# Optimization experiments

Measured on AMD Instinct MI355X. Metric: run time of the kernel, lower is better.

## Reference

```python
import jax, jax.numpy as jnp
import numpy as np

N_NODES = 50000
N_EDGES = 600000
N_FEAT = 64
D = 128
N_GRAPHS = 1024
N_LAYERS = 4


def setup_inputs() -> dict:
    key = jax.random.key(0)
    ks = jax.random.split(key, 16)
    x = jax.random.normal(ks[0], (N_NODES, N_FEAT), dtype=jnp.float32)
    edge_index = jax.random.randint(ks[1], (2, N_EDGES), 0, N_NODES, dtype=jnp.int64)
    batch_index = jnp.sort(jax.random.randint(ks[2], (N_NODES,), 0, N_GRAPHS, dtype=jnp.int64))
    def lin(k, fan_in, fan_out):
        s = 1.0 / np.sqrt(fan_in)
        kw, kb = jax.random.split(k)
        w = jax.random.uniform(kw, (fan_in, fan_out), minval=-s, maxval=s, dtype=jnp.float32)
        b = jax.random.uniform(kb, (fan_out,), minval=-s, maxval=s, dtype=jnp.float32)
        return w, b
    w0, b0 = lin(ks[3], N_FEAT, D)
    w1, b1 = lin(ks[4], D, D)
    w2, b2 = lin(ks[5], D, D)
    w3, b3 = lin(ks[6], D, D)
    wp, bp = lin(ks[7], D, D)
    return {"x": x, "edge_index": edge_index, "batch_index": batch_index,
            "w0": w0, "b0": b0, "w1": w1, "b1": b1, "w2": w2, "b2": b2,
            "w3": w3, "b3": b3, "wp": wp, "bp": bp}


def _gin_layer(x, src, dst, w, b):
    # GINConv with eps=0: MLP(x_i + sum_{j in N(i)} x_j); MLP = Linear -> ReLU
    agg = jax.ops.segment_sum(x[src], dst, num_segments=N_NODES)
    return jax.nn.relu((x + agg) @ w + b)


def reference(x, edge_index, batch_index, w0, b0, w1, b1, w2, b2, w3, b3, wp, bp):
    src, dst = edge_index[0], edge_index[1]
    # first layer changes width 64 -> 128; agg happens in input width
    agg0 = jax.ops.segment_sum(x[src], dst, num_segments=N_NODES)
    h = jax.nn.relu((x + agg0) @ w0 + b0)
    for w, b in ((w1, b1), (w2, b2), (w3, b3)):
        h = _gin_layer(h, src, dst, w, b)
    # global mean pool per graph
    sums = jax.ops.segment_sum(h, batch_index, num_segments=N_GRAPHS)
    counts = jax.ops.segment_sum(jnp.ones((N_NODES,), dtype=h.dtype), batch_index, num_segments=N_GRAPHS)
    pooled = sums / jnp.maximum(counts, 1.0)[:, None]
    # post_mp: Linear -> ReLU (dropout identity at inference)
    return jax.nn.relu(pooled @ wp + bp)
```

## Files before the change

### kernel.cpp

```cpp
#include <hip/hip_runtime.h>
#include <hip/hip_fp16.h>


#define N_NODES  50000
#define N_EDGES  600000
#define N_FEAT   64
#define DIM      128
#define N_GRAPHS 1024
#define NC       7
#define CSH      13
#define TOT2     (N_NODES * NC)
#define SCH      2048
#define NBLK     ((TOT2 + SCH - 1) / SCH)
#define TPB      256
#define GT128    ((N_NODES + 127) / 128)

typedef _Float16 f16x8 __attribute__((ext_vector_type(8)));
typedef float    f32x4 __attribute__((ext_vector_type(4)));

#define CNTZ2 (TOT2 / 4)
#define XWORK (N_NODES * N_FEAT / 4)
#define PREP_TOTAL (CNTZ2 + XWORK + N_FEAT * DIM + 3 * DIM * DIM)

__global__ __launch_bounds__(TPB) void prep_k(
    const float* __restrict__ x, __half* __restrict__ xh,
    const float* __restrict__ w0, const float* __restrict__ w1,
    const float* __restrict__ w2, const float* __restrict__ w3,
    __half* __restrict__ Wt0, __half* __restrict__ Wt1,
    __half* __restrict__ Wt2, __half* __restrict__ Wt3,
    int* __restrict__ cnt2) {
  int i = blockIdx.x * TPB + threadIdx.x;
  if (i < CNTZ2) {
    *reinterpret_cast<int4*>(cnt2 + i * 4) = make_int4(0, 0, 0, 0);
    return;
  }
  i -= CNTZ2;
  if (i < XWORK) {
    float4 v = *reinterpret_cast<const float4*>(x + (size_t)i * 4);
    union { __half2 h2[2]; uint2 u; } pk;
    pk.h2[0] = __floats2half2_rn(v.x, v.y);
    pk.h2[1] = __floats2half2_rn(v.z, v.w);
    *reinterpret_cast<uint2*>(xh + (size_t)i * 4) = pk.u;
    return;
  }
  int j = i - XWORK;
  if (j < N_FEAT * DIM) {
    int k = j >> 7, n = j & 127;
    Wt0[n * N_FEAT + k] = __float2half(w0[j]);
    return;
  }
  j -= N_FEAT * DIM;
  if (j >= 3 * DIM * DIM) return;
  int wsel = j / (DIM * DIM);
  int jj = j - wsel * (DIM * DIM);
  int k = jj >> 7, n = jj & 127;
  const float* W = (wsel == 0) ? w1 : (wsel == 1) ? w2 : w3;
  __half* Wt     = (wsel == 0) ? Wt1 : (wsel == 1) ? Wt2 : Wt3;
  Wt[n * DIM + k] = __float2half(W[jj]);
}

__global__ __launch_bounds__(TPB) void hist_k(
    const int* __restrict__ src, const int* __restrict__ dst,
    int* __restrict__ cnt2, int* __restrict__ rank) {
  int e = blockIdx.x * TPB + threadIdx.x;
  if (e >= N_EDGES) return;
  int key = dst[e] * NC + (src[e] >> CSH);
  rank[e] = atomicAdd(&cnt2[key], 1);
}

__global__ __launch_bounds__(TPB) void scan_part_k(
    const int* __restrict__ cnt2, int* __restrict__ part) {
  __shared__ int ws[4];
  int t = threadIdx.x, b = blockIdx.x;
  int base = b * SCH + t * 8;
  int s = 0;
  if (base < TOT2) {
    int4 a = *reinterpret_cast<const int4*>(cnt2 + base);
    int4 c = *reinterpret_cast<const int4*>(cnt2 + base + 4);
    s = a.x + a.y + a.z + a.w + c.x + c.y + c.z + c.w;
  }
  for (int off = 32; off; off >>= 1) s += __shfl_down(s, off, 64);
  int lane = t & 63, wv = t >> 6;
  if (lane == 0) ws[wv] = s;
  __syncthreads();
  if (t == 0) part[b] = ws[0] + ws[1] + ws[2] + ws[3];
}

__global__ __launch_bounds__(TPB) void scan_write_k(
    const int* __restrict__ cnt2, const int* __restrict__ part,
    int* __restrict__ row_ptr2) {
  __shared__ int pscan[TPB];
  __shared__ int wsum[4];
  int t = threadIdx.x, b = blockIdx.x;
  int lane = t & 63, wv = t >> 6;
  int base = b * SCH + t * 8;

  pscan[t] = (t < NBLK) ? part[t] : 0;
  __syncthreads();
  for (int off = 1; off < TPB; off <<= 1) {
    int v = (t >= off) ? pscan[t - off] : 0;
    __syncthreads();
    pscan[t] += v;
    __syncthreads();
  }
  int blk_off = (b > 0) ? pscan[b - 1] : 0;

  int v[8] = {0,0,0,0,0,0,0,0};
  if (base < TOT2) {
    int4 a = *reinterpret_cast<const int4*>(cnt2 + base);
    int4 c = *reinterpret_cast<const int4*>(cnt2 + base + 4);
    v[0]=a.x; v[1]=a.y; v[2]=a.z; v[3]=a.w;
    v[4]=c.x; v[5]=c.y; v[6]=c.z; v[7]=c.w;
  }
  int ls = 0;
#pragma unroll
  for (int i = 0; i < 8; ++i) ls += v[i];
  int incl = ls;
  for (int off = 1; off < 64; off <<= 1) {
    int u = __shfl_up(incl, off, 64);
    if (lane >= off) incl += u;
  }
  if (lane == 63) wsum[wv] = incl;
  __syncthreads();
  int woff = 0;
  for (int w = 0; w < wv; ++w) woff += wsum[w];
  int run = blk_off + woff + (incl - ls);
  if (base < TOT2) {
    int rp[8];
#pragma unroll
    for (int i = 0; i < 8; ++i) { rp[i] = run; run += v[i]; }
    *reinterpret_cast<int4*>(row_ptr2 + base) = make_int4(rp[0], rp[1], rp[2], rp[3]);
    *reinterpret_cast<int4*>(row_ptr2 + base + 4) = make_int4(rp[4], rp[5], rp[6], rp[7]);
  }
  if (b == 0 && t == 0) row_ptr2[TOT2] = N_EDGES;
}

__global__ __launch_bounds__(TPB) void fill_k(
    const int* __restrict__ src, const int* __restrict__ dst,
    const int* __restrict__ row_ptr2, const int* __restrict__ rank,
    int* __restrict__ csr_src) {
  int e = blockIdx.x * TPB + threadIdx.x;
  if (e >= N_EDGES) return;
  int s = src[e];
  int key = dst[e] * NC + (s >> CSH);
  csr_src[row_ptr2[key] + rank[e]] = s;
}

template<int K, bool EPI>
__global__ __launch_bounds__(TPB) void gemm_k(
    const __half* __restrict__ A, const __half* __restrict__ Wt,
    const float* __restrict__ bias, __half* __restrict__ y) {
  constexpr int KP = K + 8;
  constexpr int OSP = 144;
  constexpr int NKC = K / 32;
  constexpr size_t WSZ = (size_t)128 * KP * sizeof(__half);
  constexpr size_t OSZ = (size_t)128 * OSP * sizeof(__half);
  __shared__ __align__(16) char smem[WSZ > OSZ ? WSZ : OSZ];
  __half (*Ws)[KP]  = reinterpret_cast<__half(*)[KP]>(smem);
  __half (*Os)[OSP] = reinterpret_cast<__half(*)[OSP]>(smem);

  int tid = threadIdx.x;
  int w = tid >> 6, lane = tid & 63;
  int quad = lane >> 4, m = lane & 15;
  int row0 = blockIdx.x * 128;

  for (int i = tid; i < 128 * (K / 8); i += TPB) {
    int r = i / (K / 8), c = (i % (K / 8)) * 8;
    *reinterpret_cast<f16x8*>(&Ws[r][c]) =
        *reinterpret_cast<const f16x8*>(Wt + (size_t)r * K + c);
  }

  f16x8 areg[2][NKC];
#pragma unroll
  for (int s = 0; s < 2; ++s) {
    int row = row0 + w * 32 + s * 16 + m;
    row = min(row, N_NODES - 1);
    const f16x8* Ar = reinterpret_cast<const f16x8*>(A + (size_t)row * K);
#pragma unroll
    for (int kc = 0; kc < NKC; ++kc)
      areg[s][kc] = Ar[kc * 4 + quad];
  }
  __syncthreads();

  f32x4 acc[2][8];
#pragma unroll
  for (int s = 0; s < 2; ++s)
#pragma unroll
    for (int t = 0; t < 8; ++t) acc[s][t] = (f32x4){0.f, 0.f, 0.f, 0.f};

#pragma unroll
  for (int kc = 0; kc < NKC; ++kc) {
#pragma unroll
    for (int t = 0; t < 8; ++t) {
      f16x8 b = *reinterpret_cast<const f16x8*>(&Ws[t * 16 + m][kc * 32 + quad * 8]);
      acc[0][t] = __builtin_amdgcn_mfma_f32_16x16x32_f16(areg[0][kc], b, acc[0][t], 0, 0, 0);
      acc[1][t] = __builtin_amdgcn_mfma_f32_16x16x32_f16(areg[1][kc], b, acc[1][t], 0, 0, 0);
    }
  }

  __syncthreads();

#pragma unroll
  for (int t = 0; t < 8; ++t) {
    float bv = EPI ? bias[t * 16 + m] : 0.f;
#pragma unroll
    for (int s = 0; s < 2; ++s)
#pragma unroll
      for (int r = 0; r < 4; ++r) {
        float v = acc[s][t][r];
        if (EPI) v = fmaxf(v + bv, 0.f);
        Os[w * 32 + s * 16 + quad * 4 + r][t * 16 + m] = __float2half(v);
      }
  }
  __syncthreads();

#pragma unroll
  for (int it = 0; it < 8; ++it) {
    int i = tid + it * TPB;
    int r = i >> 4, c = (i & 15) * 8;
    int row = row0 + r;
    if (row < N_NODES)
      *reinterpret_cast<f16x8*>(y + (size_t)row * 128 + c) =
          *reinterpret_cast<const f16x8*>(&Os[r][c]);
  }
}

template<int F, bool BR>
__global__ __launch_bounds__(TPB) void gather_k(
    const __half* __restrict__ y, const int* __restrict__ row_ptr2,
    const int* __restrict__ csr_src, const float* __restrict__ bias,
    __half* __restrict__ hout) {
  constexpr int CH = F / 8;
  const f16x8* yv = reinterpret_cast<const f16x8*>(y);
  int gid  = blockIdx.x * TPB + threadIdx.x;
  int node = gid / CH;
  int l    = gid % CH;
  if (node >= N_NODES) return;
  int beg = row_ptr2[node * NC];
  int end = row_ptr2[node * NC + NC];

  f16x8 self = yv[(size_t)node * CH + l];
  float acc[8];
#pragma unroll
  for (int v = 0; v < 8; ++v) acc[v] = (float)self[v];

  int e = beg;
  for (; e + 3 < end; e += 4) {
    int s0 = csr_src[e+0], s1 = csr_src[e+1], s2 = csr_src[e+2], s3 = csr_src[e+3];
    f16x8 v0 = yv[(size_t)s0 * CH + l];
    f16x8 v1 = yv[(size_t)s1 * CH + l];
    f16x8 v2 = yv[(size_t)s2 * CH + l];
    f16x8 v3 = yv[(size_t)s3 * CH + l];
#pragma unroll
    for (int v = 0; v < 8; ++v)
      acc[v] += ((float)v0[v] + (float)v1[v]) + ((float)v2[v] + (float)v3[v]);
  }
  for (; e < end; ++e) {
    f16x8 v0 = yv[(size_t)csr_src[e] * CH + l];
#pragma unroll
    for (int v = 0; v < 8; ++v) acc[v] += (float)v0[v];
  }

  f16x8 o;
  if (BR) {
    float4 b0 = *reinterpret_cast<const float4*>(bias + l * 8);
    float4 b1 = *reinterpret_cast<const float4*>(bias + l * 8 + 4);
    float bb[8] = {b0.x, b0.y, b0.z, b0.w, b1.x, b1.y, b1.z, b1.w};
#pragma unroll
    for (int v = 0; v < 8; ++v) o[v] = (_Float16)fmaxf(acc[v] + bb[v], 0.f);
  } else {
#pragma unroll
    for (int v = 0; v < 8; ++v) o[v] = (_Float16)acc[v];
  }
  reinterpret_cast<f16x8*>(hout)[(size_t)node * CH + l] = o;
}

__global__ __launch_bounds__(128) void pool_post_k(
    const __half* __restrict__ h, const int* __restrict__ batch,
    const float* __restrict__ W, const float* __restrict__ bias,
    float* __restrict__ out) {
  __shared__ float xs[DIM];
  int g = blockIdx.x;
  int col = threadIdx.x;
  int lo = 0, hi = N_NODES;
  while (lo < hi) { int mid = (lo + hi) >> 1; if (batch[mid] < g) lo = mid + 1; else hi = mid; }
  int beg = lo;
  hi = N_NODES;
  while (lo < hi) { int mid = (lo + hi) >> 1; if (batch[mid] < g + 1) lo = mid + 1; else hi = mid; }
  int end = lo;

  float acc = 0.f;
  for (int n = beg; n < end; ++n) acc += __half2float(h[(size_t)n * DIM + col]);
  float cnt = fmaxf((float)(end - beg), 1.0f);
  xs[col] = acc / cnt;
  __syncthreads();
  float o = bias[col];
  for (int k = 0; k < DIM; ++k)
    o = fmaf(xs[k], W[(size_t)k * DIM + col], o);
  out[(size_t)g * DIM + col] = fmaxf(o, 0.f);
}

extern "C" void kernel_launch(void* const* d_in, const int* in_sizes, int n_in,
                              void* d_out, int out_size, void* d_ws, size_t ws_size,
                              hipStream_t stream) {
  const float* x    = (const float*)d_in[0];
  const int*   ei   = (const int*)d_in[1];
  const int*   batch= (const int*)d_in[2];
  const float* w0 = (const float*)d_in[3];  const float* b0 = (const float*)d_in[4];
  const float* w1 = (const float*)d_in[5];  const float* b1 = (const float*)d_in[6];
  const float* w2 = (const float*)d_in[7];  const float* b2 = (const float*)d_in[8];
  const float* w3 = (const float*)d_in[9];  const float* b3 = (const float*)d_in[10];
  const float* wp = (const float*)d_in[11]; const float* bp = (const float*)d_in[12];
  float* out = (float*)d_out;

  const int* src = ei;
  const int* dst = ei + N_EDGES;

  __half* xh = (__half*)d_ws;
  __half* y  = xh + (size_t)N_NODES * N_FEAT;
  __half* h  = y  + (size_t)N_NODES * DIM;
  __half* Wt0 = h + (size_t)N_NODES * DIM;
  __half* Wt1 = Wt0 + N_FEAT * DIM;
  __half* Wt2 = Wt1 + DIM * DIM;
  __half* Wt3 = Wt2 + DIM * DIM;
  int* cnt2     = (int*)(Wt3 + DIM * DIM);
  int* rank     = cnt2 + TOT2;
  int* part     = rank + N_EDGES;
  int* row_ptr2 = part + 256;
  int* csr_src  = row_ptr2 + (TOT2 + 1);
  __half* s = y;

  prep_k<<<(PREP_TOTAL + TPB - 1) / TPB, TPB, 0, stream>>>(
      x, xh, w0, w1, w2, w3, Wt0, Wt1, Wt2, Wt3, cnt2);
  hist_k<<<(N_EDGES + TPB - 1) / TPB, TPB, 0, stream>>>(src, dst, cnt2, rank);
  scan_part_k <<<NBLK, TPB, 0, stream>>>(cnt2, part);
  scan_write_k<<<NBLK, TPB, 0, stream>>>(cnt2, part, row_ptr2);
  fill_k<<<(N_EDGES + TPB - 1) / TPB, TPB, 0, stream>>>(src, dst, row_ptr2,
                                                        rank, csr_src);

  gather_k<N_FEAT, false><<<(N_NODES * 8 + TPB - 1) / TPB, TPB, 0, stream>>>(
      xh, row_ptr2, csr_src, nullptr, s);
  gemm_k<N_FEAT, true><<<GT128, TPB, 0, stream>>>(s, Wt0, b0, h);

  const __half* Wl[3] = {Wt1, Wt2, Wt3};
  const float*  Bl[3] = {b1, b2, b3};
  for (int l = 0; l < 3; ++l) {
    gemm_k<DIM, false><<<GT128, TPB, 0, stream>>>(h, Wl[l], nullptr, y);
    gather_k<DIM, true><<<(N_NODES * 16 + TPB - 1) / TPB, TPB, 0, stream>>>(
        y, row_ptr2, csr_src, Bl[l], h);
  }

  pool_post_k<<<N_GRAPHS, 128, 0, stream>>>(h, batch, wp, bp, out);
}
```

Measured before the change: 280.0 us.

## Fuse GIN gather with next layer GEMM and chain layer-0 with layer-1 GEMM

```diff
diff --git a/kernel.cpp b/kernel.cpp
--- a/kernel.cpp
+++ b/kernel.cpp
@@ -13,7 +13,7 @@
 #define SCH      2048
 #define NBLK     ((TOT2 + SCH - 1) / SCH)
 #define TPB      256
-#define GT128    ((N_NODES + 127) / 128)
+#define GT32     ((N_NODES + 31) / 32)
 
 typedef _Float16 f16x8 __attribute__((ext_vector_type(8)));
 typedef float    f32x4 __attribute__((ext_vector_type(4)));
@@ -144,85 +144,6 @@
   int s = src[e];
   int key = dst[e] * NC + (s >> CSH);
   csr_src[row_ptr2[key] + rank[e]] = s;
-}
-
-template<int K, bool EPI>
-__global__ __launch_bounds__(TPB) void gemm_k(
-    const __half* __restrict__ A, const __half* __restrict__ Wt,
-    const float* __restrict__ bias, __half* __restrict__ y) {
-  constexpr int KP = K + 8;
-  constexpr int OSP = 144;
-  constexpr int NKC = K / 32;
-  constexpr size_t WSZ = (size_t)128 * KP * sizeof(__half);
-  constexpr size_t OSZ = (size_t)128 * OSP * sizeof(__half);
-  __shared__ __align__(16) char smem[WSZ > OSZ ? WSZ : OSZ];
-  __half (*Ws)[KP]  = reinterpret_cast<__half(*)[KP]>(smem);
-  __half (*Os)[OSP] = reinterpret_cast<__half(*)[OSP]>(smem);
-
-  int tid = threadIdx.x;
-  int w = tid >> 6, lane = tid & 63;
-  int quad = lane >> 4, m = lane & 15;
-  int row0 = blockIdx.x * 128;
-
-  for (int i = tid; i < 128 * (K / 8); i += TPB) {
-    int r = i / (K / 8), c = (i % (K / 8)) * 8;
-    *reinterpret_cast<f16x8*>(&Ws[r][c]) =
-        *reinterpret_cast<const f16x8*>(Wt + (size_t)r * K + c);
-  }
-
-  f16x8 areg[2][NKC];
-#pragma unroll
-  for (int s = 0; s < 2; ++s) {
-    int row = row0 + w * 32 + s * 16 + m;
-    row = min(row, N_NODES - 1);
-    const f16x8* Ar = reinterpret_cast<const f16x8*>(A + (size_t)row * K);
-#pragma unroll
-    for (int kc = 0; kc < NKC; ++kc)
-      areg[s][kc] = Ar[kc * 4 + quad];
-  }
-  __syncthreads();
-
-  f32x4 acc[2][8];
-#pragma unroll
-  for (int s = 0; s < 2; ++s)
-#pragma unroll
-    for (int t = 0; t < 8; ++t) acc[s][t] = (f32x4){0.f, 0.f, 0.f, 0.f};
-
-#pragma unroll
-  for (int kc = 0; kc < NKC; ++kc) {
-#pragma unroll
-    for (int t = 0; t < 8; ++t) {
-      f16x8 b = *reinterpret_cast<const f16x8*>(&Ws[t * 16 + m][kc * 32 + quad * 8]);
-      acc[0][t] = __builtin_amdgcn_mfma_f32_16x16x32_f16(areg[0][kc], b, acc[0][t], 0, 0, 0);
-      acc[1][t] = __builtin_amdgcn_mfma_f32_16x16x32_f16(areg[1][kc], b, acc[1][t], 0, 0, 0);
-    }
-  }
-
-  __syncthreads();
-
-#pragma unroll
-  for (int t = 0; t < 8; ++t) {
-    float bv = EPI ? bias[t * 16 + m] : 0.f;
-#pragma unroll
-    for (int s = 0; s < 2; ++s)
-#pragma unroll
-      for (int r = 0; r < 4; ++r) {
-        float v = acc[s][t][r];
-        if (EPI) v = fmaxf(v + bv, 0.f);
-        Os[w * 32 + s * 16 + quad * 4 + r][t * 16 + m] = __float2half(v);
-      }
-  }
-  __syncthreads();
-
-#pragma unroll
-  for (int it = 0; it < 8; ++it) {
-    int i = tid + it * TPB;
-    int r = i >> 4, c = (i & 15) * 8;
-    int row = row0 + r;
-    if (row < N_NODES)
-      *reinterpret_cast<f16x8*>(y + (size_t)row * 128 + c) =
-          *reinterpret_cast<const f16x8*>(&Os[r][c]);
-  }
 }
 
 template<int F, bool BR>
@@ -275,6 +196,180 @@
   reinterpret_cast<f16x8*>(hout)[(size_t)node * CH + l] = o;
 }
 
+__global__ __launch_bounds__(TPB) void gg00_k(
+    const __half* __restrict__ s, const __half* __restrict__ Wt0,
+    const float* __restrict__ b0, const __half* __restrict__ Wt1,
+    __half* __restrict__ y1) {
+  __shared__ __align__(16) __half As[32][72];
+  __shared__ __align__(16) __half Hs[32][136];
+  int tid = threadIdx.x;
+  int row0 = blockIdx.x * 32;
+
+  {
+    int r = tid >> 3, c = (tid & 7) * 8;
+    int row = min(row0 + r, N_NODES - 1);
+    *reinterpret_cast<f16x8*>(&As[r][c]) =
+        *reinterpret_cast<const f16x8*>(s + (size_t)row * N_FEAT + c);
+  }
+  __syncthreads();
+
+  int w = tid >> 6, lane = tid & 63;
+  int quad = lane >> 4, m = lane & 15;
+  int col0 = w * 32;
+
+  f32x4 accA[2][2];
+#pragma unroll
+  for (int mt = 0; mt < 2; ++mt)
+#pragma unroll
+    for (int nt = 0; nt < 2; ++nt) accA[mt][nt] = (f32x4){0.f,0.f,0.f,0.f};
+#pragma unroll
+  for (int kc = 0; kc < 2; ++kc) {
+    f16x8 a0 = *reinterpret_cast<const f16x8*>(&As[m][kc*32 + quad*8]);
+    f16x8 a1 = *reinterpret_cast<const f16x8*>(&As[16 + m][kc*32 + quad*8]);
+#pragma unroll
+    for (int nt = 0; nt < 2; ++nt) {
+      f16x8 b = *reinterpret_cast<const f16x8*>(
+          Wt0 + (size_t)(col0 + nt*16 + m) * N_FEAT + kc*32 + quad*8);
+      accA[0][nt] = __builtin_amdgcn_mfma_f32_16x16x32_f16(a0, b, accA[0][nt], 0, 0, 0);
+      accA[1][nt] = __builtin_amdgcn_mfma_f32_16x16x32_f16(a1, b, accA[1][nt], 0, 0, 0);
+    }
+  }
+#pragma unroll
+  for (int mt = 0; mt < 2; ++mt)
+#pragma unroll
+    for (int nt = 0; nt < 2; ++nt) {
+      float bv = b0[col0 + nt*16 + m];
+#pragma unroll
+      for (int r = 0; r < 4; ++r)
+        Hs[mt*16 + quad*4 + r][col0 + nt*16 + m] =
+            __float2half(fmaxf(accA[mt][nt][r] + bv, 0.f));
+    }
+  __syncthreads();
+
+  f32x4 accB[2][2];
+#pragma unroll
+  for (int mt = 0; mt < 2; ++mt)
+#pragma unroll
+    for (int nt = 0; nt < 2; ++nt) accB[mt][nt] = (f32x4){0.f,0.f,0.f,0.f};
+#pragma unroll
+  for (int kc = 0; kc < 4; ++kc) {
+    f16x8 a0 = *reinterpret_cast<const f16x8*>(&Hs[m][kc*32 + quad*8]);
+    f16x8 a1 = *reinterpret_cast<const f16x8*>(&Hs[16 + m][kc*32 + quad*8]);
+#pragma unroll
+    for (int nt = 0; nt < 2; ++nt) {
+      f16x8 b = *reinterpret_cast<const f16x8*>(
+          Wt1 + (size_t)(col0 + nt*16 + m) * DIM + kc*32 + quad*8);
+      accB[0][nt] = __builtin_amdgcn_mfma_f32_16x16x32_f16(a0, b, accB[0][nt], 0, 0, 0);
+      accB[1][nt] = __builtin_amdgcn_mfma_f32_16x16x32_f16(a1, b, accB[1][nt], 0, 0, 0);
+    }
+  }
+  __syncthreads();
+#pragma unroll
+  for (int mt = 0; mt < 2; ++mt)
+#pragma unroll
+    for (int nt = 0; nt < 2; ++nt)
+#pragma unroll
+      for (int r = 0; r < 4; ++r)
+        Hs[mt*16 + quad*4 + r][col0 + nt*16 + m] = __float2half(accB[mt][nt][r]);
+  __syncthreads();
+#pragma unroll
+  for (int it = 0; it < 2; ++it) {
+    int i = tid + it * TPB;
+    int r = i >> 4, c = (i & 15) * 8;
+    int row = row0 + r;
+    if (row < N_NODES)
+      *reinterpret_cast<f16x8*>(y1 + (size_t)row * DIM + c) =
+          *reinterpret_cast<const f16x8*>(&Hs[r][c]);
+  }
+}
+
+__global__ __launch_bounds__(TPB) void fgg_k(
+    const __half* __restrict__ y, const int* __restrict__ row_ptr2,
+    const int* __restrict__ csr_src, const float* __restrict__ bias,
+    const __half* __restrict__ Wn, __half* __restrict__ yout) {
+  __shared__ __align__(16) __half As[32][136];
+  const f16x8* yv = reinterpret_cast<const f16x8*>(y);
+  int tid = threadIdx.x;
+  int row0 = blockIdx.x * 32;
+  int g = tid >> 4, l = tid & 15;
+
+#pragma unroll 1
+  for (int p = 0; p < 2; ++p) {
+    int node = row0 + p * 16 + g;
+    if (node < N_NODES) {
+      int beg = row_ptr2[node * NC];
+      int end = row_ptr2[node * NC + NC];
+      f16x8 self = yv[(size_t)node * 16 + l];
+      float acc[8];
+#pragma unroll
+      for (int v = 0; v < 8; ++v) acc[v] = (float)self[v];
+      int e = beg;
+      for (; e + 3 < end; e += 4) {
+        int s0 = csr_src[e+0], s1 = csr_src[e+1], s2 = csr_src[e+2], s3 = csr_src[e+3];
+        f16x8 v0 = yv[(size_t)s0 * 16 + l];
+        f16x8 v1 = yv[(size_t)s1 * 16 + l];
+        f16x8 v2 = yv[(size_t)s2 * 16 + l];
+        f16x8 v3 = yv[(size_t)s3 * 16 + l];
+#pragma unroll
+        for (int v = 0; v < 8; ++v)
+          acc[v] += ((float)v0[v] + (float)v1[v]) + ((float)v2[v] + (float)v3[v]);
+      }
+      for (; e < end; ++e) {
+        f16x8 v0 = yv[(size_t)csr_src[e] * 16 + l];
+#pragma unroll
+        for (int v = 0; v < 8; ++v) acc[v] += (float)v0[v];
+      }
+      float4 bb0 = *reinterpret_cast<const float4*>(bias + l * 8);
+      float4 bb1 = *reinterpret_cast<const float4*>(bias + l * 8 + 4);
+      float bb[8] = {bb0.x, bb0.y, bb0.z, bb0.w, bb1.x, bb1.y, bb1.z, bb1.w};
+      f16x8 o;
+#pragma unroll
+      for (int v = 0; v < 8; ++v) o[v] = (_Float16)fmaxf(acc[v] + bb[v], 0.f);
+      *reinterpret_cast<f16x8*>(&As[p * 16 + g][l * 8]) = o;
+    }
+  }
+  __syncthreads();
+
+  int w = tid >> 6, lane = tid & 63;
+  int quad = lane >> 4, m = lane & 15;
+  int col0 = w * 32;
+  f32x4 acc2[2][2];
+#pragma unroll
+  for (int mt = 0; mt < 2; ++mt)
+#pragma unroll
+    for (int nt = 0; nt < 2; ++nt) acc2[mt][nt] = (f32x4){0.f,0.f,0.f,0.f};
+#pragma unroll
+  for (int kc = 0; kc < 4; ++kc) {
+    f16x8 a0 = *reinterpret_cast<const f16x8*>(&As[m][kc*32 + quad*8]);
+    f16x8 a1 = *reinterpret_cast<const f16x8*>(&As[16 + m][kc*32 + quad*8]);
+#pragma unroll
+    for (int nt = 0; nt < 2; ++nt) {
+      f16x8 b = *reinterpret_cast<const f16x8*>(
+          Wn + (size_t)(col0 + nt*16 + m) * DIM + kc*32 + quad*8);
+      acc2[0][nt] = __builtin_amdgcn_mfma_f32_16x16x32_f16(a0, b, acc2[0][nt], 0, 0, 0);
+      acc2[1][nt] = __builtin_amdgcn_mfma_f32_16x16x32_f16(a1, b, acc2[1][nt], 0, 0, 0);
+    }
+  }
+  __syncthreads();
+#pragma unroll
+  for (int mt = 0; mt < 2; ++mt)
+#pragma unroll
+    for (int nt = 0; nt < 2; ++nt)
+#pragma unroll
+      for (int r = 0; r < 4; ++r)
+        As[mt*16 + quad*4 + r][col0 + nt*16 + m] = __float2half(acc2[mt][nt][r]);
+  __syncthreads();
+#pragma unroll
+  for (int it = 0; it < 2; ++it) {
+    int i = tid + it * TPB;
+    int r = i >> 4, c = (i & 15) * 8;
+    int row = row0 + r;
+    if (row < N_NODES)
+      *reinterpret_cast<f16x8*>(yout + (size_t)row * DIM + c) =
+          *reinterpret_cast<const f16x8*>(&As[r][c]);
+  }
+}
+
 __global__ __launch_bounds__(128) void pool_post_k(
     const __half* __restrict__ h, const int* __restrict__ batch,
     const float* __restrict__ W, const float* __restrict__ bias,
@@ -317,8 +412,10 @@
   const int* dst = ei + N_EDGES;
 
   __half* xh = (__half*)d_ws;
-  __half* y  = xh + (size_t)N_NODES * N_FEAT;
-  __half* h  = y  + (size_t)N_NODES * DIM;
+  __half* sb = xh + (size_t)N_NODES * N_FEAT;
+  __half* yA = sb + (size_t)N_NODES * N_FEAT;
+  __half* yB = yA + (size_t)N_NODES * DIM;
+  __half* h  = yB + (size_t)N_NODES * DIM;
   __half* Wt0 = h + (size_t)N_NODES * DIM;
   __half* Wt1 = Wt0 + N_FEAT * DIM;
   __half* Wt2 = Wt1 + DIM * DIM;
@@ -328,7 +425,6 @@
   int* part     = rank + N_EDGES;
   int* row_ptr2 = part + 256;
   int* csr_src  = row_ptr2 + (TOT2 + 1);
-  __half* s = y;
 
   prep_k<<<(PREP_TOTAL + TPB - 1) / TPB, TPB, 0, stream>>>(
       x, xh, w0, w1, w2, w3, Wt0, Wt1, Wt2, Wt3, cnt2);
@@ -339,16 +435,15 @@
                                                         rank, csr_src);
 
   gather_k<N_FEAT, false><<<(N_NODES * 8 + TPB - 1) / TPB, TPB, 0, stream>>>(
-      xh, row_ptr2, csr_src, nullptr, s);
-  gemm_k<N_FEAT, true><<<GT128, TPB, 0, stream>>>(s, Wt0, b0, h);
-
-  const __half* Wl[3] = {Wt1, Wt2, Wt3};
-  const float*  Bl[3] = {b1, b2, b3};
-  for (int l = 0; l < 3; ++l) {
-    gemm_k<DIM, false><<<GT128, TPB, 0, stream>>>(h, Wl[l], nullptr, y);
-    gather_k<DIM, true><<<(N_NODES * 16 + TPB - 1) / TPB, TPB, 0, stream>>>(
-        y, row_ptr2, csr_src, Bl[l], h);
-  }
+      xh, row_ptr2, csr_src, nullptr, sb);
+
+  gg00_k<<<GT32, TPB, 0, stream>>>(sb, Wt0, b0, Wt1, yA);
+
+  fgg_k<<<GT32, TPB, 0, stream>>>(yA, row_ptr2, csr_src, b1, Wt2, yB);
+  fgg_k<<<GT32, TPB, 0, stream>>>(yB, row_ptr2, csr_src, b2, Wt3, yA);
+
+  gather_k<DIM, true><<<(N_NODES * 16 + TPB - 1) / TPB, TPB, 0, stream>>>(
+      yA, row_ptr2, csr_src, b3, h);
 
   pool_post_k<<<N_GRAPHS, 128, 0, stream>>>(h, batch, wp, bp, out);
 }
```

After: 263.3 us. 6.0% less time.
